# Optimization experiments

Measured on AMD Instinct MI355X. Metric: run time of the kernel, lower is better.

The kernel has to match this reference:

```python
import jax, jax.numpy as jnp
import numpy as np

H = 4
N = 50000
D_IN = 128
D_MODEL = 256
NCLASS = 40
B_S = 1
BH = B_S * H
LN_EPS = 1e-5


def sparse_perm_1D(indices, values, feats, n, bh):
    """Batched sparse (bh,n,n) @ dense (bh,n,d): gather -> scale -> segment-sum scatter."""
    gathered = feats[indices[0], indices[2]]              # (nnz, d)
    contrib = values[:, None] * gathered                   # (nnz, d)
    seg = indices[0] * n + indices[1]                      # (nnz,)
    out = jax.ops.segment_sum(contrib, seg, num_segments=bh * n)
    return out.reshape(bh, n, -1)


def layer_norm(x, gamma, beta):
    mu = jnp.mean(x, axis=-1, keepdims=True)
    var = jnp.var(x, axis=-1, keepdims=True)
    return (x - mu) * jax.lax.rsqrt(var + LN_EPS) * gamma + beta


def setup_inputs() -> dict:
    key = jax.random.key(0)
    k1, k2, k3, k4, k5, k6, k7 = jax.random.split(key, 7)
    # per-(batch*head) permutation sigma: nonzero at (b, i, sigma_b(i))
    perm_keys = jax.random.split(k1, BH)
    sigma = jax.vmap(lambda k: jax.random.permutation(k, N))(perm_keys)  # (BH, N)
    b_idx = jnp.repeat(jnp.arange(BH), N)
    row_idx = jnp.tile(jnp.arange(N), BH)
    col_idx = sigma.reshape(-1)
    perm_indices = jnp.stack([b_idx, row_idx, col_idx], axis=0).astype(jnp.int32)  # (3, BH*N)
    perm_values = jax.random.uniform(k2, (BH * N,), dtype=jnp.float32)
    features = jax.random.normal(k3, (B_S, N, D_IN), dtype=jnp.float32)
    appd = jax.random.normal(k4, (B_S, N, D_IN), dtype=jnp.float32)
    # parameters
    w_scale_in = 1.0 / np.sqrt(2 * D_IN)
    W_in = jax.random.uniform(k5, (2 * D_IN, D_MODEL), dtype=jnp.float32, minval=-w_scale_in, maxval=w_scale_in)
    b_in = jnp.zeros((D_MODEL,), dtype=jnp.float32)
    ln_gamma = jnp.ones((D_MODEL * H,), dtype=jnp.float32)
    ln_beta = jnp.zeros((D_MODEL * H,), dtype=jnp.float32)
    w_scale_h = 1.0 / np.sqrt(D_MODEL * H)
    W_head = jax.random.uniform(k6, (D_MODEL * H, NCLASS), dtype=jnp.float32, minval=-w_scale_h, maxval=w_scale_h)
    b_head = jax.random.uniform(k7, (NCLASS,), dtype=jnp.float32, minval=-w_scale_h, maxval=w_scale_h)
    return {"perm_indices": perm_indices, "perm_values": perm_values,
            "features": features, "appd": appd,
            "W_in": W_in, "b_in": b_in,
            "ln_gamma": ln_gamma, "ln_beta": ln_beta,
            "W_head": W_head, "b_head": b_head}


def reference(perm_indices, perm_values, features, appd, W_in, b_in, ln_gamma, ln_beta, W_head, b_head):
    # concat auxiliary features, replicate per head: (B_S,N,2*D_IN) -> (BH,N,2*D_IN)
    feat = jnp.concatenate([features, appd], axis=-1)
    feat = jnp.broadcast_to(feat[:, None], (B_S, H, N, 2 * D_IN)).reshape(BH, N, 2 * D_IN)
    # permute rows: perm @ feat
    x = sparse_perm_1D(perm_indices, perm_values, feat, N, BH)
    # ff_in + relu (dropout is identity at eval)
    x = jax.nn.relu(x @ W_in + b_in)                       # (BH, N, D_MODEL)
    # nlayers == nblocks == 0: compress/uncompress loops are empty
    # inverse permutation: perm^T @ x (swap row/col indices)
    idx_t = jnp.stack([perm_indices[0], perm_indices[2], perm_indices[1]], axis=0)
    y = sparse_perm_1D(idx_t, perm_values, x, N, BH)       # (BH, N, D_MODEL)
    # (B_S,H,N,D) -> (B_S,N,H*D)
    y = y.reshape(B_S, H, N, D_MODEL).transpose(0, 2, 1, 3).reshape(B_S, N, H * D_MODEL)
    y = layer_norm(y, ln_gamma, ln_beta)
    return y @ W_head + b_head                             # (B_S, N, NCLASS)
```

## Files before the change

### kernel.cpp

```cpp
#include <hip/hip_runtime.h>
#include <hip/hip_bf16.h>

#define NROW 50000
#define DIN 128
#define DM 256
#define HH 4
#define NC 40
#define BHN 200000
#define NBLK 782

typedef float f32x4 __attribute__((ext_vector_type(4)));
typedef short bf16x8 __attribute__((ext_vector_type(8)));

__device__ __forceinline__ unsigned int pk2(float lo, float hi) {
    __hip_bfloat162 h = __float22bfloat162_rn(make_float2(lo, hi));
    return *(unsigned int*)&h;
}

__device__ __forceinline__ void gl_lds16(const unsigned short* g, unsigned short* l) {
    __builtin_amdgcn_global_load_lds(
        (const __attribute__((address_space(1))) unsigned int*)(g),
        (__attribute__((address_space(3))) unsigned int*)(l),
        16, 0, 0);
}

__global__ __launch_bounds__(256) void k_prep(const int* __restrict__ pi,
                                              const float* __restrict__ pv,
                                              const float* __restrict__ Win,
                                              const float* __restrict__ Wh,
                                              const float* __restrict__ gamma,
                                              const float* __restrict__ beta,
                                              const float* __restrict__ bh,
                                              float* __restrict__ vcol,
                                              unsigned short* __restrict__ Wpk,
                                              unsigned short* __restrict__ Wgpk,
                                              float* __restrict__ bias2,
                                              float* __restrict__ wsum) {
    const int bid = blockIdx.x, tid = threadIdx.x;
    if (bid < 196) {
        int k4 = (bid * 256 + tid) * 4;
        if (k4 < BHN) {
            int4   c4 = *(const int4*)&pi[2 * BHN + k4];
            float4 v4 = *(const float4*)&pv[k4];
            int b = (k4 >= 150000) ? 3 : (k4 >= 100000) ? 2 : (k4 >= 50000) ? 1 : 0;
            float* vb = vcol + b * NROW;
            vb[c4.x] = v4.x; vb[c4.y] = v4.y; vb[c4.z] = v4.z; vb[c4.w] = v4.w;
        }
    } else if (bid < 212) {
        int base = (bid - 196) * 512;
        #pragma unroll
        for (int qq = 0; qq < 2; ++qq) {
            int s = base + qq * 256 + tid;
            int ln = s & 63;
            int t  = (s >> 6) & 15;
            int kc = s >> 10;
            int n  = t * 16 + (ln & 15);
            int kb = kc * 32 + ((ln >> 4) << 3);
            union { unsigned int ui[4]; uint4 v4; } u;
            #pragma unroll
            for (int jj = 0; jj < 4; ++jj)
                u.ui[jj] = pk2(Win[(kb + 2 * jj) * DM + n], Win[(kb + 2 * jj + 1) * DM + n]);
            *(uint4*)&Wpk[s * 8] = u.v4;
        }
    } else if (bid < 224) {
        int base = (bid - 212) * 512;
        #pragma unroll
        for (int qq = 0; qq < 2; ++qq) {
            int s = base + qq * 256 + tid;
            int ln = s & 63;
            int u6 = s >> 6;
            int t  = u6 % 3;
            int v6 = u6 / 3;
            int kc = v6 & 7;
            int h  = v6 >> 3;
            int c  = t * 16 + (ln & 15);
            int dbase = h * 256 + kc * 32 + ((ln >> 4) << 2);
            union { unsigned int ui[4]; uint4 v4; } u;
            if (c < NC) {
                #pragma unroll
                for (int jj = 0; jj < 4; ++jj) {
                    int dA = dbase + ((jj >> 1) << 4) + ((jj & 1) << 1);
                    u.ui[jj] = pk2(gamma[dA] * Wh[dA * NC + c],
                                   gamma[dA + 1] * Wh[(dA + 1) * NC + c]);
                }
            } else {
                u.v4 = make_uint4(0u, 0u, 0u, 0u);
            }
            *(uint4*)&Wgpk[s * 8] = u.v4;
        }
    } else {
        __shared__ float redb[256], redw[256];
        int c = bid - 224;
        float sb = 0.f, sw = 0.f;
        #pragma unroll
        for (int q = 0; q < 4; ++q) {
            int d = tid + 256 * q;
            float w = Wh[d * NC + c];
            sb = fmaf(beta[d], w, sb);
            sw = fmaf(gamma[d], w, sw);
        }
        redb[tid] = sb; redw[tid] = sw;
        __syncthreads();
        for (int st = 128; st > 0; st >>= 1) {
            if (tid < st) { redb[tid] += redb[tid + st]; redw[tid] += redw[tid + st]; }
            __syncthreads();
        }
        if (tid == 0) { bias2[c] = bh[c] + redb[0]; wsum[c] = redw[0]; }
    }
}

#define Y_PASS(H, HALF) { \
    const float vh = vm[H]; \
    _Pragma("unroll") \
    for (int tt = 0; tt < 8; ++tt) { \
        float4 b4 = *(const float4*)&bshm[((HALF) * 8 + tt) * 16 + quad * 4]; \
        float y0 = vh * fmaxf(fmaf(vh, accG[tt][0], b4.x), 0.f); \
        float y1 = vh * fmaxf(fmaf(vh, accG[tt][1], b4.y), 0.f); \
        float y2 = vh * fmaxf(fmaf(vh, accG[tt][2], b4.z), 0.f); \
        float y3 = vh * fmaxf(fmaf(vh, accG[tt][3], b4.w), 0.f); \
        s_ += (y0 + y1) + (y2 + y3); \
        ss_ = fmaf(y0, y0, ss_); ss_ = fmaf(y1, y1, ss_); \
        ss_ = fmaf(y2, y2, ss_); ss_ = fmaf(y3, y3, ss_); \
        ya[tt * 2]     = pk2(y0, y1); \
        ya[tt * 2 + 1] = pk2(y2, y3); \
    } }

#define HEAD_MFMA(H) { \
    _Pragma("unroll") \
    for (int kcl = 0; kcl < 4; ++kcl) { \
        union { unsigned int ui[4]; bf16x8 v; } af; \
        af.ui[0] = ya[4 * kcl];     af.ui[1] = ya[4 * kcl + 1]; \
        af.ui[2] = ya[4 * kcl + 2]; af.ui[3] = ya[4 * kcl + 3]; \
        _Pragma("unroll") \
        for (int t3 = 0; t3 < 3; ++t3) { \
            bf16x8 wf = *(const bf16x8*)&stage[((((H) & 1) * 12 + kcl * 3 + t3) * 64 + ln) * 8]; \
            accO[t3] = __builtin_amdgcn_mfma_f32_16x16x32_bf16(af.v, wf, accO[t3], 0, 0, 0); \
        } } }

__global__ __launch_bounds__(256, 3) void k_fused(
    const float* __restrict__ feats, const float* __restrict__ appd,
    const unsigned short* __restrict__ Wpk,
    const unsigned short* __restrict__ Wgpk,
    const float* __restrict__ vcol,
    const float* __restrict__ b_in,
    const float* __restrict__ bias2,
    const float* __restrict__ wsum,
    float* __restrict__ out)
{
    __shared__ __align__(16) unsigned short stage[16384];
    __shared__ __align__(16) float bshm[256];

    const int tid = threadIdx.x;
    const int wv = tid >> 6;
    const int ln = tid & 63;
    const int quad = ln >> 4;
    const int lr = ln & 15;
    const int jw = blockIdx.x * 64 + wv * 16;
    const int ar = min(jw + lr, NROW - 1);

    #pragma unroll
    for (int q = 0; q < 4; ++q) {
        int f = wv * 4 + q;
        gl_lds16(Wpk + ((size_t)(((f >> 3) * 16 + (f & 7)) * 64 + ln)) * 8, &stage[f * 512]);
    }
    bshm[tid] = b_in[tid];

    float vm[HH];
    #pragma unroll
    for (int h = 0; h < HH; ++h) vm[h] = vcol[h * NROW + ar];

    const f32x4 zero4 = {0.f, 0.f, 0.f, 0.f};
    float s_ = 0.f, ss_ = 0.f;
    f32x4 accO[3];
    #pragma unroll
    for (int t = 0; t < 3; ++t) accO[t] = zero4;
    f32x4 accG[8];
    unsigned int ya[16];

    #pragma unroll
    for (int half = 0; half < 2; ++half) {
        if (half == 1) asm volatile("" ::: "memory");

        unsigned int afr[8][4];
        {
            const float* rf = feats + (size_t)ar * DIN;
            const float* ra = appd  + (size_t)ar * DIN;
            #pragma unroll
            for (int kc = 0; kc < 8; ++kc) {
                const float* src = (kc < 4) ? rf : ra;
                const int ko = (kc & 3) * 32 + quad * 8;
                float4 x0 = *(const float4*)(src + ko);
                float4 x1 = *(const float4*)(src + ko + 4);
                afr[kc][0] = pk2(x0.x, x0.y);
                afr[kc][1] = pk2(x0.z, x0.w);
                afr[kc][2] = pk2(x1.x, x1.y);
                afr[kc][3] = pk2(x1.z, x1.w);
            }
        }

        #pragma unroll
        for (int c = 0; c < 4; ++c) {
            __syncthreads();
            if (c < 3) {
                #pragma unroll
                for (int q = 0; q < 4; ++q) {
                    int f = wv * 4 + q;
                    int kc = 2 * (c + 1) + (f >> 3), th = f & 7;
                    gl_lds16(Wpk + ((size_t)((kc * 16 + half * 8 + th) * 64 + ln)) * 8,
                             &stage[((c + 1) & 1) * 8192 + f * 512]);
                }
            }
            #pragma unroll
            for (int kcl = 0; kcl < 2; ++kcl) {
                union { unsigned int ui[4]; bf16x8 v; } a;
                a.ui[0] = afr[2 * c + kcl][0]; a.ui[1] = afr[2 * c + kcl][1];
                a.ui[2] = afr[2 * c + kcl][2]; a.ui[3] = afr[2 * c + kcl][3];
                #pragma unroll
                for (int th = 0; th < 8; ++th) {
                    bf16x8 wf = *(const bf16x8*)&stage[(c & 1) * 8192 + ((kcl * 8 + th) * 64 + ln) * 8];
                    accG[th] = __builtin_amdgcn_mfma_f32_16x16x32_bf16(
                        wf, a.v, (c == 0 && kcl == 0) ? zero4 : accG[th], 0, 0, 0);
                }
            }
        }
        __syncthreads();

        #pragma unroll
        for (int hp = 0; hp < 2; ++hp) {
            #pragma unroll
            for (int q = 0; q < 6; ++q) {
                int f = wv * 6 + q;
                int hl = f / 12, rem = f % 12, kcr = rem / 3, t3 = rem % 3;
                int h = 2 * hp + hl;
                gl_lds16(Wgpk + ((size_t)(((h * 8 + half * 4 + kcr) * 3 + t3) * 64 + ln)) * 8,
                         &stage[f * 512]);
            }
            if (hp == 0) { Y_PASS(0, half) } else { Y_PASS(2, half) }
            __syncthreads();
            if (hp == 0) {
                HEAD_MFMA(0)
                Y_PASS(1, half)
                HEAD_MFMA(1)
            } else {
                HEAD_MFMA(2)
                Y_PASS(3, half)
                HEAD_MFMA(3)
            }
            __syncthreads();
        }
        if (half == 0) {
            #pragma unroll
            for (int q = 0; q < 4; ++q) {
                int f = wv * 4 + q;
                gl_lds16(Wpk + ((size_t)(((f >> 3) * 16 + 8 + (f & 7)) * 64 + ln)) * 8,
                         &stage[f * 512]);
            }
        }
    }

    s_  += __shfl_xor(s_, 16);  s_  += __shfl_xor(s_, 32);
    ss_ += __shfl_xor(ss_, 16); ss_ += __shfl_xor(ss_, 32);
    float mm  = s_ * (1.f / 1024.f);
    float var = ss_ * (1.f / 1024.f) - mm * mm;
    float rs  = rsqrtf(var + 1e-5f);
    float nm  = -mm * rs;

    float rs_r[4], nm_r[4];
    #pragma unroll
    for (int rg = 0; rg < 4; ++rg) {
        int rloc = quad * 4 + rg;
        rs_r[rg] = __shfl(rs, rloc);
        nm_r[rg] = __shfl(nm, rloc);
    }
    #pragma unroll
    for (int t = 0; t < 3; ++t) {
        int c = t * 16 + lr;
        if (c < NC) {
            float w2 = wsum[c], b2 = bias2[c];
            #pragma unroll
            for (int rg = 0; rg < 4; ++rg) {
                int row = jw + quad * 4 + rg;
                if (row < NROW)
                    out[(size_t)row * NC + c] = fmaf(rs_r[rg], accO[t][rg], fmaf(nm_r[rg], w2, b2));
            }
        }
    }
}

extern "C" void kernel_launch(void* const* d_in, const int* in_sizes, int n_in,
                              void* d_out, int out_size, void* d_ws, size_t ws_size,
                              hipStream_t stream) {
    const int*   pi    = (const int*)d_in[0];
    const float* pv    = (const float*)d_in[1];
    const float* feats = (const float*)d_in[2];
    const float* appd  = (const float*)d_in[3];
    const float* Win   = (const float*)d_in[4];
    const float* b_in  = (const float*)d_in[5];
    const float* gamma = (const float*)d_in[6];
    const float* beta  = (const float*)d_in[7];
    const float* Wh    = (const float*)d_in[8];
    const float* bh    = (const float*)d_in[9];
    float* out = (float*)d_out;

    char* w = (char*)d_ws;
    float*          vcolW  = (float*)w;
    unsigned short* WpkW   = (unsigned short*)(w + 800000);
    unsigned short* WgpkW  = (unsigned short*)(w + 931072);
    float*          bias2W = (float*)(w + 1029376);
    float*          wsumW  = (float*)(w + 1029536);

    k_prep<<<264, 256, 0, stream>>>(pi, pv, Win, Wh, gamma, beta, bh,
                                    vcolW, WpkW, WgpkW, bias2W, wsumW);
    k_fused<<<NBLK, 256, 0, stream>>>(feats, appd, WpkW, WgpkW, vcolW, b_in,
                                      bias2W, wsumW, out);
}
```

Baseline: 146.7 us.

## Load weight fragments directly from global into registers instead of LDS staging

Removes the double-buffered LDS staging of the packed input and head weights, along with its global_load_lds async copies and the many __syncthreads barriers between stages. Each wave now reads its bf16 weight fragments straight from global memory (L2/L1-resident) into registers just before its MFMAs. This frees about 32KB of LDS per block and removes block-wide synchronisation. In exchange every wave re-fetches the same weights through the cache hierarchy, adds vector-register pressure, and loses the explicit prefetch overlap.

```diff
diff --git a/kernel.cpp b/kernel.cpp
--- a/kernel.cpp
+++ b/kernel.cpp
@@ -15,13 +15,6 @@
 __device__ __forceinline__ unsigned int pk2(float lo, float hi) {
     __hip_bfloat162 h = __float22bfloat162_rn(make_float2(lo, hi));
     return *(unsigned int*)&h;
-}
-
-__device__ __forceinline__ void gl_lds16(const unsigned short* g, unsigned short* l) {
-    __builtin_amdgcn_global_load_lds(
-        (const __attribute__((address_space(1))) unsigned int*)(g),
-        (__attribute__((address_space(3))) unsigned int*)(l),
-        16, 0, 0);
 }
 
 __global__ __launch_bounds__(256) void k_prep(const int* __restrict__ pi,
@@ -125,18 +118,6 @@
         ya[tt * 2 + 1] = pk2(y2, y3); \
     } }
 
-#define HEAD_MFMA(H) { \
-    _Pragma("unroll") \
-    for (int kcl = 0; kcl < 4; ++kcl) { \
-        union { unsigned int ui[4]; bf16x8 v; } af; \
-        af.ui[0] = ya[4 * kcl];     af.ui[1] = ya[4 * kcl + 1]; \
-        af.ui[2] = ya[4 * kcl + 2]; af.ui[3] = ya[4 * kcl + 3]; \
-        _Pragma("unroll") \
-        for (int t3 = 0; t3 < 3; ++t3) { \
-            bf16x8 wf = *(const bf16x8*)&stage[((((H) & 1) * 12 + kcl * 3 + t3) * 64 + ln) * 8]; \
-            accO[t3] = __builtin_amdgcn_mfma_f32_16x16x32_bf16(af.v, wf, accO[t3], 0, 0, 0); \
-        } } }
-
 __global__ __launch_bounds__(256, 3) void k_fused(
     const float* __restrict__ feats, const float* __restrict__ appd,
     const unsigned short* __restrict__ Wpk,
@@ -147,7 +128,6 @@
     const float* __restrict__ wsum,
     float* __restrict__ out)
 {
-    __shared__ __align__(16) unsigned short stage[16384];
     __shared__ __align__(16) float bshm[256];
 
     const int tid = threadIdx.x;
@@ -158,16 +138,15 @@
     const int jw = blockIdx.x * 64 + wv * 16;
     const int ar = min(jw + lr, NROW - 1);
 
-    #pragma unroll
-    for (int q = 0; q < 4; ++q) {
-        int f = wv * 4 + q;
-        gl_lds16(Wpk + ((size_t)(((f >> 3) * 16 + (f & 7)) * 64 + ln)) * 8, &stage[f * 512]);
-    }
     bshm[tid] = b_in[tid];
+    __syncthreads();
 
     float vm[HH];
     #pragma unroll
     for (int h = 0; h < HH; ++h) vm[h] = vcol[h * NROW + ar];
+
+    const unsigned short* wpL = Wpk  + (size_t)ln * 8;
+    const unsigned short* wgL = Wgpk + (size_t)ln * 8;
 
     const f32x4 zero4 = {0.f, 0.f, 0.f, 0.f};
     float s_ = 0.f, ss_ = 0.f;
@@ -199,61 +178,39 @@
         }
 
         #pragma unroll
-        for (int c = 0; c < 4; ++c) {
-            __syncthreads();
-            if (c < 3) {
+        for (int kc = 0; kc < 8; ++kc) {
+            union { unsigned int ui[4]; bf16x8 v; } a;
+            a.ui[0] = afr[kc][0]; a.ui[1] = afr[kc][1];
+            a.ui[2] = afr[kc][2]; a.ui[3] = afr[kc][3];
+            bf16x8 wf[8];
+            #pragma unroll
+            for (int th = 0; th < 8; ++th)
+                wf[th] = *(const bf16x8*)&wpL[(size_t)(kc * 16 + half * 8 + th) * 512];
+            #pragma unroll
+            for (int th = 0; th < 8; ++th)
+                accG[th] = __builtin_amdgcn_mfma_f32_16x16x32_bf16(
+                    wf[th], a.v, (kc == 0) ? zero4 : accG[th], 0, 0, 0);
+        }
+
+        #pragma unroll
+        for (int h = 0; h < HH; ++h) {
+            bf16x8 wg[12];
+            #pragma unroll
+            for (int kcr = 0; kcr < 4; ++kcr)
                 #pragma unroll
-                for (int q = 0; q < 4; ++q) {
-                    int f = wv * 4 + q;
-                    int kc = 2 * (c + 1) + (f >> 3), th = f & 7;
-                    gl_lds16(Wpk + ((size_t)((kc * 16 + half * 8 + th) * 64 + ln)) * 8,
-                             &stage[((c + 1) & 1) * 8192 + f * 512]);
-                }
-            }
-            #pragma unroll
-            for (int kcl = 0; kcl < 2; ++kcl) {
-                union { unsigned int ui[4]; bf16x8 v; } a;
-                a.ui[0] = afr[2 * c + kcl][0]; a.ui[1] = afr[2 * c + kcl][1];
-                a.ui[2] = afr[2 * c + kcl][2]; a.ui[3] = afr[2 * c + kcl][3];
+                for (int t3 = 0; t3 < 3; ++t3)
+                    wg[kcr * 3 + t3] = *(const bf16x8*)
+                        &wgL[(size_t)(((h * 8 + half * 4 + kcr) * 3 + t3)) * 512];
+            Y_PASS(h, half)
+            #pragma unroll
+            for (int kcr = 0; kcr < 4; ++kcr) {
+                union { unsigned int ui[4]; bf16x8 v; } af;
+                af.ui[0] = ya[4 * kcr];     af.ui[1] = ya[4 * kcr + 1];
+                af.ui[2] = ya[4 * kcr + 2]; af.ui[3] = ya[4 * kcr + 3];
                 #pragma unroll
-                for (int th = 0; th < 8; ++th) {
-                    bf16x8 wf = *(const bf16x8*)&stage[(c & 1) * 8192 + ((kcl * 8 + th) * 64 + ln) * 8];
-                    accG[th] = __builtin_amdgcn_mfma_f32_16x16x32_bf16(
-                        wf, a.v, (c == 0 && kcl == 0) ? zero4 : accG[th], 0, 0, 0);
-                }
-            }
-        }
-        __syncthreads();
-
-        #pragma unroll
-        for (int hp = 0; hp < 2; ++hp) {
-            #pragma unroll
-            for (int q = 0; q < 6; ++q) {
-                int f = wv * 6 + q;
-                int hl = f / 12, rem = f % 12, kcr = rem / 3, t3 = rem % 3;
-                int h = 2 * hp + hl;
-                gl_lds16(Wgpk + ((size_t)(((h * 8 + half * 4 + kcr) * 3 + t3) * 64 + ln)) * 8,
-                         &stage[f * 512]);
-            }
-            if (hp == 0) { Y_PASS(0, half) } else { Y_PASS(2, half) }
-            __syncthreads();
-            if (hp == 0) {
-                HEAD_MFMA(0)
-                Y_PASS(1, half)
-                HEAD_MFMA(1)
-            } else {
-                HEAD_MFMA(2)
-                Y_PASS(3, half)
-                HEAD_MFMA(3)
-            }
-            __syncthreads();
-        }
-        if (half == 0) {
-            #pragma unroll
-            for (int q = 0; q < 4; ++q) {
-                int f = wv * 4 + q;
-                gl_lds16(Wpk + ((size_t)(((f >> 3) * 16 + 8 + (f & 7)) * 64 + ln)) * 8,
-                         &stage[f * 512]);
+                for (int t3 = 0; t3 < 3; ++t3)
+                    accO[t3] = __builtin_amdgcn_mfma_f32_16x16x32_bf16(
+                        af.v, wg[kcr * 3 + t3], accO[t3], 0, 0, 0);
             }
         }
     }
```

Result: slower. 170.2 us (+16.0%).
